# Kernel tuning notes

Measured on AMD Instinct MI355X. Metric: run time of the kernel, lower is better.

## Reference

```python
import jax, jax.numpy as jnp
import numpy as np

D_MODEL = 1024
N_HEADS = 16
HEAD_DIM = D_MODEL // N_HEADS


def setup_inputs() -> dict:
    key = jax.random.key(0)
    ks = jax.random.split(key, 6)
    B, S = 2, 2048
    scale = 1.0 / np.sqrt(D_MODEL)
    x = jax.random.normal(ks[0], (B, S, D_MODEL), dtype=jnp.float32)
    Wq = jax.random.normal(ks[1], (D_MODEL, D_MODEL), dtype=jnp.float32) * scale
    Wk = jax.random.normal(ks[2], (D_MODEL, D_MODEL), dtype=jnp.float32) * scale
    Wv = jax.random.normal(ks[3], (D_MODEL, D_MODEL), dtype=jnp.float32) * scale
    Wo = jax.random.normal(ks[4], (D_MODEL, D_MODEL), dtype=jnp.float32) * scale
    bo = jax.random.normal(ks[5], (D_MODEL,), dtype=jnp.float32) * 0.02
    return {"x": x, "Wq": Wq, "Wk": Wk, "Wv": Wv, "Wo": Wo, "bo": bo}


def reference(x, Wq, Wk, Wv, Wo, bo):
    B, S, _ = x.shape
    H, hd = N_HEADS, HEAD_DIM
    # qkv projections (no bias, qkv_bias=False)
    q = (x @ Wq).reshape(B, S, H, hd).transpose(0, 2, 1, 3)  # [B,H,S,hd]
    k = (x @ Wk).reshape(B, S, H, hd).transpose(0, 2, 1, 3)
    v = (x @ Wv).reshape(B, S, H, hd).transpose(0, 2, 1, 3)
    scores = jnp.einsum('bhqd,bhkd->bhqk', q, k)  # [B,H,S,S]
    causal = jnp.tril(jnp.ones((S, S), dtype=bool))  # True = keep
    scores = jnp.where(causal, scores, -jnp.inf)
    weights = jax.nn.softmax(scores / np.sqrt(hd), axis=-1)
    # dropout p=0.0 -> identity
    ctx = jnp.einsum('bhqk,bhkd->bhqd', weights, v)  # [B,H,S,hd]
    ctx = ctx.transpose(0, 2, 1, 3).reshape(B, S, H * hd)
    return ctx @ Wo + bo
```

## Files before the change

kernel.cpp:

```cpp
#include <hip/hip_runtime.h>
#include <hip/hip_bf16.h>
#include <stdint.h>

#define SEQ    2048
#define BATCH  2
#define DMODEL 1024
#define NHEADS 16
#define HDIM   64
#define MROWS  (BATCH*SEQ)

typedef __attribute__((ext_vector_type(8))) short bf16x8;
typedef __attribute__((ext_vector_type(4))) float f32x4;

__device__ inline void global_to_lds16(const void* g, void* l) {
  __builtin_amdgcn_global_load_lds(
      (const __attribute__((address_space(1))) uint32_t*)g,
      (__attribute__((address_space(3))) uint32_t*)l, 16, 0, 0);
}

__device__ inline unsigned short f2bf_bits(float f) {
  __hip_bfloat16 h = __float2bfloat16(f);
  return *(unsigned short*)&h;
}

__global__ void cvt_x(const float* __restrict__ x, __hip_bfloat16* __restrict__ xb) {
  int i = (blockIdx.x * 256 + threadIdx.x) * 4;
  float4 v = *(const float4*)(x + i);
  ushort4 o;
  o.x = f2bf_bits(v.x); o.y = f2bf_bits(v.y);
  o.z = f2bf_bits(v.z); o.w = f2bf_bits(v.w);
  *(ushort4*)(xb + i) = o;
}

__global__ void trans_w(const float* __restrict__ Wq, const float* __restrict__ Wk,
                        const float* __restrict__ Wv, const float* __restrict__ Wo,
                        __hip_bfloat16* __restrict__ Wqkv_t, __hip_bfloat16* __restrict__ Wo_t) {
  __shared__ float tile[32][33];
  int z = blockIdx.z;
  const float* W = (z == 0) ? Wq : (z == 1) ? Wk : (z == 2) ? Wv : Wo;
  __hip_bfloat16* dst = (z < 3) ? (Wqkv_t + (size_t)z * 1024 * 1024) : Wo_t;
  int k0 = blockIdx.x * 32, n0 = blockIdx.y * 32;
  int tx = threadIdx.x & 31, ty = threadIdx.x >> 5;
#pragma unroll
  for (int r = 0; r < 4; r++)
    tile[ty + r * 8][tx] = W[(size_t)(k0 + ty + r * 8) * 1024 + n0 + tx];
  __syncthreads();
#pragma unroll
  for (int r = 0; r < 4; r++)
    dst[(size_t)(n0 + ty + r * 8) * 1024 + k0 + tx] = __float2bfloat16(tile[tx][ty + r * 8]);
}

__global__ void trans_v(const __hip_bfloat16* __restrict__ QKV, __hip_bfloat16* __restrict__ Vt) {
  __shared__ __hip_bfloat16 tile[64][72];
  int bh = blockIdx.y;
  int b = bh >> 4, h = bh & 15;
  int s0 = blockIdx.x * 64;
  int t = threadIdx.x;
  int r = t >> 2, cg = (t & 3) * 16;
  const __hip_bfloat16* src = QKV + ((size_t)(b * SEQ + s0 + r)) * 3072 + 2048 + h * 64 + cg;
  *(uint4*)&tile[r][cg]     = *(const uint4*)src;
  *(uint4*)&tile[r][cg + 8] = *(const uint4*)(src + 8);
  __syncthreads();
  unsigned short tmp[16];
#pragma unroll
  for (int i = 0; i < 16; i++) tmp[i] = *(const unsigned short*)&tile[cg + i][r];
  __hip_bfloat16* dst = Vt + ((size_t)bh * 64 + r) * 2048 + s0 + cg;
  *(uint4*)dst       = *(const uint4*)&tmp[0];
  *(uint4*)(dst + 8) = *(const uint4*)&tmp[8];
}

template <int TN, bool OUT_BF16, int MINW>
__global__ __launch_bounds__(256, MINW)
void gemm_kernel(const __hip_bfloat16* __restrict__ A, const __hip_bfloat16* __restrict__ Bt,
                 void* __restrict__ C, const float* __restrict__ bias, int ldc) {
  __shared__ __hip_bfloat16 Asl[128 * 32];
  __shared__ __hip_bfloat16 Bsl[TN * 32];

  const int t = threadIdx.x;
  const int lane = t & 63;
  const int w = t >> 6;
  constexpr int MI = (TN == 128) ? 4 : 2;
  const int wrow = (TN == 128) ? (w >> 1) * 64 : w * 32;
  const int wcol = (TN == 128) ? (w & 1) * 64 : 0;
  const int m0 = blockIdx.y * 128;
  const int n0 = blockIdx.x * TN;

  f32x4 acc[MI][4];
#pragma unroll
  for (int i = 0; i < MI; i++)
#pragma unroll
    for (int j = 0; j < 4; j++) acc[i][j] = (f32x4){0.f, 0.f, 0.f, 0.f};

  const int rA0 = w * 16 + (lane >> 2);
  const int kof = (lane & 3) * 8;
  const int fm = lane & 15;
  const int fk = (lane >> 4) * 8;

  for (int k0 = 0; k0 < 1024; k0 += 32) {
#pragma unroll
    for (int i = 0; i < 2; i++) {
      int r = rA0 + i * 64;
      global_to_lds16(A + (size_t)(m0 + r) * 1024 + k0 + kof, (void*)(Asl + r * 32 + kof));
    }
#pragma unroll
    for (int i = 0; i < TN / 64; i++) {
      int r = rA0 + i * 64;
      global_to_lds16(Bt + (size_t)(n0 + r) * 1024 + k0 + kof, (void*)(Bsl + r * 32 + kof));
    }
    __syncthreads();
    bf16x8 af[MI], bfr[4];
#pragma unroll
    for (int mi = 0; mi < MI; mi++)
      af[mi] = *(const bf16x8*)(Asl + (wrow + mi * 16 + fm) * 32 + fk);
#pragma unroll
    for (int ni = 0; ni < 4; ni++)
      bfr[ni] = *(const bf16x8*)(Bsl + (wcol + ni * 16 + fm) * 32 + fk);
#pragma unroll
    for (int mi = 0; mi < MI; mi++)
#pragma unroll
      for (int ni = 0; ni < 4; ni++)
        acc[mi][ni] = __builtin_amdgcn_mfma_f32_16x16x32_bf16(af[mi], bfr[ni], acc[mi][ni], 0, 0, 0);
    __syncthreads();
  }

#pragma unroll
  for (int mi = 0; mi < MI; mi++) {
    int mb = m0 + wrow + mi * 16 + (lane >> 4) * 4;
#pragma unroll
    for (int ni = 0; ni < 4; ni++) {
      int n = n0 + wcol + ni * 16 + fm;
      float bv = OUT_BF16 ? 0.f : bias[n];
#pragma unroll
      for (int r = 0; r < 4; r++) {
        if (OUT_BF16)
          ((__hip_bfloat16*)C)[(size_t)(mb + r) * ldc + n] = __float2bfloat16(acc[mi][ni][r]);
        else
          ((float*)C)[(size_t)(mb + r) * ldc + n] = acc[mi][ni][r] + bv;
      }
    }
  }
}

__global__ __launch_bounds__(256, 2)
void attn_kernel(const __hip_bfloat16* __restrict__ QKV,
                 const __hip_bfloat16* __restrict__ Vt,
                 __hip_bfloat16* __restrict__ ctx) {
  __shared__ __hip_bfloat16 Klds[128 * 64];
  __shared__ __hip_bfloat16 Vlds[64 * 128];
  __shared__ __hip_bfloat16 Plds[2][64 * 72];

  const int t = threadIdx.x;
  const int lane = t & 63;
  const int w = t >> 6;
  const int jb = blockIdx.x;
  const int qtab[2] = { jb, 31 - jb };
  const int bh = blockIdx.y;
  const int b = bh >> 4, h = bh & 15;
  const int fm = lane & 15;
  const int g4 = lane >> 4;
  const int fk = g4 * 8;
  const size_t rowb = (size_t)b * SEQ;
  const float c = 0.18033688011112042f;

  const int krr = lane >> 3;
  const int kjc = (lane & 7) ^ krr;
  const int vrr = lane >> 4;
  const int vjc = (lane & 15) ^ vrr;

  bf16x8 qf[2][2];
#pragma unroll
  for (int hh = 0; hh < 2; hh++) {
    const __hip_bfloat16* qp = QKV + (rowb + qtab[hh] * 64 + w * 16 + fm) * 3072 + h * 64 + fk;
    bf16x8 r0 = *(const bf16x8*)qp;
    bf16x8 r1 = *(const bf16x8*)(qp + 32);
#pragma unroll
    for (int i = 0; i < 8; i++) {
      float f0 = __uint_as_float(((unsigned)(unsigned short)r0[i]) << 16) * c;
      float f1 = __uint_as_float(((unsigned)(unsigned short)r1[i]) << 16) * c;
      r0[i] = (short)f2bf_bits(f0);
      r1[i] = (short)f2bf_bits(f1);
    }
    qf[hh][0] = r0; qf[hh][1] = r1;
  }

  bf16x8 ones;
#pragma unroll
  for (int i = 0; i < 8; i++) ones[i] = (short)0x3F80;

  f32x4 acc[2][4];
  f32x4 lacc[2];
#pragma unroll
  for (int hh = 0; hh < 2; hh++) {
    lacc[hh] = (f32x4){0.f, 0.f, 0.f, 0.f};
#pragma unroll
    for (int d = 0; d < 4; d++) acc[hh][d] = (f32x4){0.f, 0.f, 0.f, 0.f};
  }

  const int lastt = qtab[1] >> 1;
  for (int ktt2 = 0; ktt2 <= lastt; ++ktt2) {
    const int kt0 = ktt2 * 128;
    __syncthreads();
#pragma unroll
    for (int i = 0; i < 4; i++) {
      int seg = w + i * 4;
      int kr = seg * 8 + krr;
      global_to_lds16(QKV + (rowb + kt0 + kr) * 3072 + 1024 + h * 64 + kjc * 8,
                      (void*)(Klds + seg * 512 + lane * 8));
      int vr = seg * 4 + vrr;
      global_to_lds16(Vt + ((size_t)bh * 64 + vr) * 2048 + kt0 + vjc * 8,
                      (void*)(Vlds + seg * 512 + lane * 8));
    }
    __syncthreads();

#pragma unroll
    for (int sc = 0; sc < 2; sc++) {
      const int kts = ktt2 * 2 + sc;
#pragma unroll
      for (int hh = 0; hh < 2; hh++) {
        if (kts > qtab[hh]) continue;
        f32x4 s[4];
#pragma unroll
        for (int ns = 0; ns < 4; ns++) s[ns] = (f32x4){0.f, 0.f, 0.f, 0.f};
#pragma unroll
        for (int kk = 0; kk < 2; kk++) {
#pragma unroll
          for (int ns = 0; ns < 4; ns++) {
            int row = sc * 64 + ns * 16 + fm;
            bf16x8 kf = *(const bf16x8*)(Klds + row * 64 + (((kk * 4 + g4) ^ (fm & 7)) << 3));
            s[ns] = __builtin_amdgcn_mfma_f32_16x16x32_bf16(qf[hh][kk], kf, s[ns], 0, 0, 0);
          }
        }
        const bool diag = (kts == qtab[hh]);
        __hip_bfloat16* P = (__hip_bfloat16*)Plds[hh];
#pragma unroll
        for (int ns = 0; ns < 4; ns++)
#pragma unroll
          for (int r = 0; r < 4; r++) {
            bool msk = diag && (ns * 16 + fm > w * 16 + g4 * 4 + r);
            float p = msk ? 0.f : exp2f(s[ns][r]);
            P[(w * 16 + g4 * 4 + r) * 72 + ns * 16 + fm] = __float2bfloat16(p);
          }
#pragma unroll
        for (int kk = 0; kk < 2; kk++) {
          bf16x8 pa = *(const bf16x8*)(P + (w * 16 + fm) * 72 + kk * 32 + fk);
          lacc[hh] = __builtin_amdgcn_mfma_f32_16x16x32_bf16(pa, ones, lacc[hh], 0, 0, 0);
#pragma unroll
          for (int dd = 0; dd < 4; dd++) {
            int vslot = (sc * 8 + kk * 4 + g4) ^ (fm & 3);
            bf16x8 vf = *(const bf16x8*)(Vlds + (dd * 16 + fm) * 128 + vslot * 8);
            acc[hh][dd] = __builtin_amdgcn_mfma_f32_16x16x32_bf16(pa, vf, acc[hh][dd], 0, 0, 0);
          }
        }
      }
    }
  }

#pragma unroll
  for (int hh = 0; hh < 2; hh++) {
#pragma unroll
    for (int dd = 0; dd < 4; dd++)
#pragma unroll
      for (int r = 0; r < 4; r++) {
        int q = qtab[hh] * 64 + w * 16 + g4 * 4 + r;
        ctx[(rowb + q) * 1024 + h * 64 + dd * 16 + fm] =
            __float2bfloat16(acc[hh][dd][r] / lacc[hh][r]);
      }
  }
}

extern "C" void kernel_launch(void* const* d_in, const int* in_sizes, int n_in,
                              void* d_out, int out_size, void* d_ws, size_t ws_size,
                              hipStream_t stream) {
  const float* x  = (const float*)d_in[0];
  const float* Wq = (const float*)d_in[1];
  const float* Wk = (const float*)d_in[2];
  const float* Wv = (const float*)d_in[3];
  const float* Wo = (const float*)d_in[4];
  const float* bo = (const float*)d_in[5];
  float* out = (float*)d_out;

  char* ws = (char*)d_ws;
  __hip_bfloat16* xb     = (__hip_bfloat16*)(ws);
  __hip_bfloat16* Wqkv_t = (__hip_bfloat16*)(ws + (8ull  << 20));
  __hip_bfloat16* Wo_t   = (__hip_bfloat16*)(ws + (14ull << 20));
  __hip_bfloat16* QKV    = (__hip_bfloat16*)(ws + (16ull << 20));
  __hip_bfloat16* ctxb   = (__hip_bfloat16*)(ws + (40ull << 20));
  __hip_bfloat16* Vt     = xb;

  cvt_x<<<dim3(MROWS * DMODEL / (256 * 4)), dim3(256), 0, stream>>>(x, xb);
  trans_w<<<dim3(32, 32, 4), dim3(256), 0, stream>>>(Wq, Wk, Wv, Wo, Wqkv_t, Wo_t);
  gemm_kernel<128, true, 3><<<dim3(24, 32), dim3(256), 0, stream>>>(xb, Wqkv_t, (void*)QKV, nullptr, 3072);
  trans_v<<<dim3(32, 32), dim3(256), 0, stream>>>(QKV, Vt);
  attn_kernel<<<dim3(16, 32), dim3(256), 0, stream>>>(QKV, Vt, ctxb);
  gemm_kernel<64, false, 2><<<dim3(16, 32), dim3(256), 0, stream>>>(ctxb, Wo_t, (void*)out, bo, 1024);
}
```

Measured before the change: 196.0 us.

## Double-buffer K/V tiles in LDS to overlap loads with attention compute

The attention kernel now keeps two K and V LDS buffers. It prefetches the next 128-key tile with async global-to-LDS loads while computing on the current one, and drops one of the two barriers per iteration. To make room, the P scratch is cut to a single buffer shared by both query halves, and the V swizzle is widened to use 8 slots. It also switches to the hardware exp2 and reciprocal builtins in the softmax and normalization. The cost is more LDS per block (about 73KB), which may strain two-blocks-per-CU occupancy, plus slightly lower-precision exp and reciprocal.

```diff
diff --git a/kernel.cpp b/kernel.cpp
--- a/kernel.cpp
+++ b/kernel.cpp
@@ -145,9 +145,9 @@
 void attn_kernel(const __hip_bfloat16* __restrict__ QKV,
                  const __hip_bfloat16* __restrict__ Vt,
                  __hip_bfloat16* __restrict__ ctx) {
-  __shared__ __hip_bfloat16 Klds[128 * 64];
-  __shared__ __hip_bfloat16 Vlds[64 * 128];
-  __shared__ __hip_bfloat16 Plds[2][64 * 72];
+  __shared__ __hip_bfloat16 Klds[2][128 * 64];
+  __shared__ __hip_bfloat16 Vlds[2][64 * 128];
+  __shared__ __hip_bfloat16 Plds[64 * 72];
 
   const int t = threadIdx.x;
   const int lane = t & 63;
@@ -165,7 +165,7 @@
   const int krr = lane >> 3;
   const int kjc = (lane & 7) ^ krr;
   const int vrr = lane >> 4;
-  const int vjc = (lane & 15) ^ vrr;
+  const int vjc = (lane & 15) ^ ((w & 1) * 4 + vrr);
 
   bf16x8 qf[2][2];
 #pragma unroll
@@ -196,21 +196,27 @@
     for (int d = 0; d < 4; d++) acc[hh][d] = (f32x4){0.f, 0.f, 0.f, 0.f};
   }
 
-  const int lastt = qtab[1] >> 1;
-  for (int ktt2 = 0; ktt2 <= lastt; ++ktt2) {
+  auto stage = [&](int ktt2, int bufi) {
     const int kt0 = ktt2 * 128;
-    __syncthreads();
 #pragma unroll
     for (int i = 0; i < 4; i++) {
       int seg = w + i * 4;
       int kr = seg * 8 + krr;
       global_to_lds16(QKV + (rowb + kt0 + kr) * 3072 + 1024 + h * 64 + kjc * 8,
-                      (void*)(Klds + seg * 512 + lane * 8));
+                      (void*)(&Klds[bufi][0] + seg * 512 + lane * 8));
       int vr = seg * 4 + vrr;
       global_to_lds16(Vt + ((size_t)bh * 64 + vr) * 2048 + kt0 + vjc * 8,
-                      (void*)(Vlds + seg * 512 + lane * 8));
-    }
+                      (void*)(&Vlds[bufi][0] + seg * 512 + lane * 8));
+    }
+  };
+
+  const int lastt = qtab[1] >> 1;
+  stage(0, 0);
+  for (int ktt2 = 0; ktt2 <= lastt; ++ktt2) {
     __syncthreads();
+    if (ktt2 < lastt) stage(ktt2 + 1, (ktt2 + 1) & 1);
+    const __hip_bfloat16* Kb = &Klds[ktt2 & 1][0];
+    const __hip_bfloat16* Vb = &Vlds[ktt2 & 1][0];
 
 #pragma unroll
     for (int sc = 0; sc < 2; sc++) {
@@ -226,28 +232,27 @@
 #pragma unroll
           for (int ns = 0; ns < 4; ns++) {
             int row = sc * 64 + ns * 16 + fm;
-            bf16x8 kf = *(const bf16x8*)(Klds + row * 64 + (((kk * 4 + g4) ^ (fm & 7)) << 3));
+            bf16x8 kf = *(const bf16x8*)(Kb + row * 64 + (((kk * 4 + g4) ^ (fm & 7)) << 3));
             s[ns] = __builtin_amdgcn_mfma_f32_16x16x32_bf16(qf[hh][kk], kf, s[ns], 0, 0, 0);
           }
         }
         const bool diag = (kts == qtab[hh]);
-        __hip_bfloat16* P = (__hip_bfloat16*)Plds[hh];
 #pragma unroll
         for (int ns = 0; ns < 4; ns++)
 #pragma unroll
           for (int r = 0; r < 4; r++) {
             bool msk = diag && (ns * 16 + fm > w * 16 + g4 * 4 + r);
-            float p = msk ? 0.f : exp2f(s[ns][r]);
-            P[(w * 16 + g4 * 4 + r) * 72 + ns * 16 + fm] = __float2bfloat16(p);
+            float p = msk ? 0.f : __builtin_amdgcn_exp2f(s[ns][r]);
+            Plds[(w * 16 + g4 * 4 + r) * 72 + ns * 16 + fm] = __float2bfloat16(p);
           }
 #pragma unroll
         for (int kk = 0; kk < 2; kk++) {
-          bf16x8 pa = *(const bf16x8*)(P + (w * 16 + fm) * 72 + kk * 32 + fk);
+          bf16x8 pa = *(const bf16x8*)(Plds + (w * 16 + fm) * 72 + kk * 32 + fk);
           lacc[hh] = __builtin_amdgcn_mfma_f32_16x16x32_bf16(pa, ones, lacc[hh], 0, 0, 0);
 #pragma unroll
           for (int dd = 0; dd < 4; dd++) {
-            int vslot = (sc * 8 + kk * 4 + g4) ^ (fm & 3);
-            bf16x8 vf = *(const bf16x8*)(Vlds + (dd * 16 + fm) * 128 + vslot * 8);
+            int vslot = (sc * 8 + kk * 4 + g4) ^ (fm & 7);
+            bf16x8 vf = *(const bf16x8*)(Vb + (dd * 16 + fm) * 128 + vslot * 8);
             acc[hh][dd] = __builtin_amdgcn_mfma_f32_16x16x32_bf16(pa, vf, acc[hh][dd], 0, 0, 0);
           }
         }
@@ -257,13 +262,16 @@
 
 #pragma unroll
   for (int hh = 0; hh < 2; hh++) {
+    float rl[4];
+#pragma unroll
+    for (int r = 0; r < 4; r++) rl[r] = __builtin_amdgcn_rcpf(lacc[hh][r]);
 #pragma unroll
     for (int dd = 0; dd < 4; dd++)
 #pragma unroll
       for (int r = 0; r < 4; r++) {
         int q = qtab[hh] * 64 + w * 16 + g4 * 4 + r;
         ctx[(rowb + q) * 1024 + h * 64 + dd * 16 + fm] =
-            __float2bfloat16(acc[hh][dd][r] / lacc[hh][r]);
+            __float2bfloat16(acc[hh][dd][r] * rl[r]);
       }
   }
 }
```

Result: faster. 189.0 us (-3.6%).
